# Performance work log

Hardware: AMD Instinct MI355X
Metric: run time of the kernel (lower is better)

The kernel has to match this reference:

```python
import jax, jax.numpy as jnp
import numpy as np
from math import factorial

LMAX = 4
L2 = (LMAX + 1) ** 2                      # 25 spherical components
RES_B = 2 * (2 * LMAX + 1)                # 18 Gauss-Legendre beta nodes (exact for band 2*lmax products)
RES_A = 2 * (2 * LMAX + 1) + 1            # 19 uniform alpha nodes
EPS = 1e-5
# degree index of each (l,m) slot: [0,1,1,1,2,...]
L_IDX = np.repeat(np.arange(LMAX + 1), 2 * np.arange(LMAX + 1) + 1)


def _assoc_legendre(lmax, x):
    # Associated Legendre P_l^m(x) with Condon-Shortley phase; returns [l, m, B]
    B = x.shape[0]
    P = np.zeros((lmax + 1, lmax + 1, B))
    P[0, 0] = 1.0
    sx = np.sqrt(np.maximum(0.0, 1.0 - x * x))
    for m in range(1, lmax + 1):
        P[m, m] = -(2 * m - 1) * sx * P[m - 1, m - 1]
    for m in range(lmax):
        P[m + 1, m] = (2 * m + 1) * x * P[m, m]
    for m in range(lmax + 1):
        for l in range(m + 2, lmax + 1):
            P[l, m] = ((2 * l - 1) * x * P[l - 1, m] - (l + m - 1) * P[l - 2, m]) / (l - m)
    return P


def _build_sh(lmax, res_b, res_a):
    # Real orthonormal spherical harmonics sampled on a Gauss-Legendre x uniform-phi grid.
    ct, wb = np.polynomial.legendre.leggauss(res_b)       # cos(theta) nodes / weights
    phi = np.arange(res_a) * (2.0 * np.pi / res_a)
    P = _assoc_legendre(lmax, ct)
    l2 = (lmax + 1) ** 2
    Y = np.zeros((res_b, res_a, l2))
    for l in range(lmax + 1):
        for m in range(l + 1):
            Nlm = np.sqrt((2 * l + 1) / (4.0 * np.pi) * factorial(l - m) / factorial(l + m))
            if m == 0:
                Y[:, :, l * l + l] = (Nlm * P[l, 0])[:, None]
            else:
                base = np.sqrt(2.0) * Nlm * P[l, m]
                Y[:, :, l * l + l + m] = base[:, None] * np.cos(m * phi)[None, :]
                Y[:, :, l * l + l - m] = base[:, None] * np.sin(m * phi)[None, :]
    w = (wb[:, None] * np.full((1, res_a), 2.0 * np.pi / res_a)).reshape(-1)
    Yf = Y.reshape(-1, l2)
    return Yf, w

_Y_np, _w_np = _build_sh(LMAX, RES_B, RES_A)
TO_GRID = jnp.asarray(_Y_np, dtype=jnp.float32)                     # [G, L2]
FROM_GRID = jnp.asarray((_w_np[:, None] * _Y_np).T, dtype=jnp.float32)  # [L2, G], exact SH projection


def setup_inputs() -> dict:
    key = jax.random.key(0)
    ks = jax.random.split(key, 8)
    N, C = 6000, 128
    x = jax.random.normal(ks[0], (N, L2, C), dtype=jnp.float32)
    batch = jax.random.randint(ks[1], (N,), 0, 77)
    s = 1.0 / np.sqrt(C)
    return {
        "x": x,
        "batch": batch,
        "norm_w": jnp.ones((LMAX + 1, C), dtype=jnp.float32),
        "norm_b": jnp.zeros((C,), dtype=jnp.float32),
        "w1": jax.random.normal(ks[2], (LMAX + 1, C, C), dtype=jnp.float32) * s,
        "b1": jax.random.normal(ks[3], (C,), dtype=jnp.float32) * 0.02,
        "w_tp": jax.random.normal(ks[4], (LMAX + 1, C), dtype=jnp.float32),
        "w2": jax.random.normal(ks[5], (LMAX + 1, C, C), dtype=jnp.float32) * s,
        "b2": jax.random.normal(ks[6], (C,), dtype=jnp.float32) * 0.02,
    }


def _merge_layer_norm(x, w, b):
    # x: [N, L2, C]; center l=0 over channels, RMS over all components+channels, per-(l,C) affine.
    mean0 = jnp.mean(x[:, 0:1, :], axis=-1, keepdims=True)
    xc = jnp.concatenate([x[:, 0:1, :] - mean0, x[:, 1:, :]], axis=1)
    var = jnp.mean(xc * xc, axis=(1, 2), keepdims=True)
    xn = xc * jax.lax.rsqrt(var + EPS)
    out = xn * w[L_IDX][None]                      # [N, L2, C]
    return jnp.concatenate([out[:, 0:1, :] + b, out[:, 1:, :]], axis=1)


def _so3_linear(x, w, b):
    # per-degree linear: w [lmax+1, out, in]; bias on l=0 only
    W = w[L_IDX]                                    # [L2, out, in]
    y = jnp.einsum('nlc,lkc->nlk', x, W)
    return jnp.concatenate([y[:, 0:1, :] + b, y[:, 1:, :]], axis=1)


def _gaunt_self_tp(x, w_tp):
    # Gaunt self tensor-product (depthwise): pointwise square on the sphere,
    # exact projection back to SH (Gaunt-coefficient contraction), per-(l,C) weight.
    g = jnp.einsum('nlc,gl->ngc', x, TO_GRID)       # [N, G, C] to-grid
    y = jnp.einsum('ngc,lg->nlc', g * g, FROM_GRID)  # [N, L2, C] from-grid
    return y * w_tp[L_IDX][None]


def reference(x, batch, norm_w, norm_b, w1, b1, w_tp, w2, b2):
    x_res = x
    h = _merge_layer_norm(x, norm_w, norm_b)
    h = _so3_linear(h, w1, b1)
    h = _gaunt_self_tp(h, w_tp)
    h = _so3_linear(h, w2, b2)
    return h + x_res  # ffn_shortcut is Identity (num_in == num_out)
```

## Files before the change

### kernel.cpp

```cpp
#include <hip/hip_runtime.h>
#include <math.h>

#define L2C 25
#define CH  128
#define NB  16
#define GLB 7
#define GLA 13
#define NG  91
#define GPAD 96
#define KPAD 32
#define HROWS 401

typedef short bf16x8 __attribute__((ext_vector_type(8)));
typedef int   i32x4  __attribute__((ext_vector_type(4)));
typedef float f32x4  __attribute__((ext_vector_type(4)));
typedef unsigned uint2v __attribute__((ext_vector_type(2)));

union frag_u { i32x4 i; bf16x8 h; };

__device__ inline short f2bf(float f) {
  union { float f; unsigned u; } v; v.f = f;
  unsigned r = (v.u + 0x7FFFu + ((v.u >> 16) & 1u)) >> 16;
  return (short)r;
}
__device__ inline unsigned cvt_pk_bf16(float lo, float hi) {
  unsigned r; asm("v_cvt_pk_bf16_f32 %0, %1, %2" : "=v"(r) : "v"(lo), "v"(hi)); return r;
}

__global__ void build_tables_kernel(short* __restrict__ toT, short* __restrict__ frT) {
  const int g = threadIdx.x;
  if (g >= GPAD) return;
  const double PI = 3.14159265358979323846;
  double Y[L2C];
  double wg = 0.0;
  if (g < NG) {
    const int b = g / GLA;
    const int a = g % GLA;
    double xx = cos(PI * (b + 0.75) / (GLB + 0.5));
    double pp = 1.0;
    for (int it = 0; it < 64; ++it) {
      double p0 = 1.0, p1 = xx;
      for (int j = 2; j <= GLB; ++j) { double p2 = ((2.0*j-1.0)*xx*p1 - (j-1.0)*p0)/j; p0 = p1; p1 = p2; }
      pp = GLB * (xx*p1 - p0) / (xx*xx - 1.0);
      xx -= p1 / pp;
    }
    { double p0 = 1.0, p1 = xx;
      for (int j = 2; j <= GLB; ++j) { double p2 = ((2.0*j-1.0)*xx*p1 - (j-1.0)*p0)/j; p0 = p1; p1 = p2; }
      pp = GLB * (xx*p1 - p0) / (xx*xx - 1.0); }
    const double wb = 2.0 / ((1.0 - xx*xx) * pp * pp);
    const double ct = xx;
    const double sx = sqrt(fmax(0.0, 1.0 - ct*ct));
    double P[5][5];
    P[0][0] = 1.0;
    for (int m = 1; m <= 4; ++m) P[m][m] = -(2.0*m - 1.0) * sx * P[m-1][m-1];
    for (int m = 0; m <= 3; ++m) P[m+1][m] = (2.0*m + 1.0) * ct * P[m][m];
    for (int m = 0; m <= 4; ++m)
      for (int l = m + 2; l <= 4; ++l)
        P[l][m] = ((2.0*l-1.0)*ct*P[l-1][m] - (l+m-1.0)*P[l-2][m]) / (l - m);
    const double fact[9] = {1,1,2,6,24,120,720,5040,40320};
    const double phi = (2.0*PI/GLA) * a;
    for (int l = 0; l <= 4; ++l)
      for (int m = 0; m <= l; ++m) {
        double Nlm = sqrt((2.0*l+1.0)/(4.0*PI) * fact[l-m]/fact[l+m]);
        if (m == 0) Y[l*l + l] = Nlm * P[l][0];
        else {
          double base = sqrt(2.0) * Nlm * P[l][m];
          Y[l*l + l + m] = base * cos((double)m * phi);
          Y[l*l + l - m] = base * sin((double)m * phi);
        }
      }
    wg = wb * (2.0*PI/GLA);
  }
  for (int l = 0; l < KPAD; ++l) {
    float tv = (g < NG && l < L2C) ? (float)Y[l] : 0.f;
    toT[g*KPAD + l] = f2bf(tv);
  }
  {
    const int hi = g >> 4, r = g & 15;
    const int ksv = hi >> 1, pa = hi & 1;
    const int lqv = r >> 2,  pb = r & 3;
    const int kg = ksv*32 + lqv*8 + pa*4 + pb;
    for (int l = 0; l < KPAD; ++l)
      frT[l*GPAD + kg] = (g < NG && l < L2C) ? f2bf((float)(wg * Y[l])) : (short)0;
  }
}

__global__ void convert_w_kernel(const float* __restrict__ w1, const float* __restrict__ w2,
                                 short* __restrict__ wb1, short* __restrict__ wb2) {
  const int i = blockIdx.x * 256 + threadIdx.x;
  if (i < 5*CH*CH) { wb1[i] = f2bf(w1[i]); wb2[i] = f2bf(w2[i]); }
}

__global__ __launch_bounds__(512, 2) void eqv3_fused16(
    const float* __restrict__ x,
    const float* __restrict__ norm_w, const float* __restrict__ norm_b,
    const short* __restrict__ wb1, const float* __restrict__ b1,
    const float* __restrict__ w_tp,
    const short* __restrict__ wb2, const float* __restrict__ b2,
    const short* __restrict__ toT, const short* __restrict__ frT,
    float* __restrict__ out)
{
  __shared__ __align__(16) short u[65536];
  short (*hsh)[HROWS][8] = (short (*)[HROWS][8])u;
  short (*hg)[4][CH][8]  = (short (*)[4][CH][8])u;

  const int tid  = threadIdx.x;
  const int w    = tid >> 6;
  const int lane = tid & 63;
  const int l16  = lane & 15;
  const int lq   = lane >> 4;
  const long n0  = (long)blockIdx.x * NB;
  const int k    = w*16 + l16;

  constexpr int LDEG[L2C] = {0,1,1,1,2,2,2,2,2,3,3,3,3,3,3,3,4,4,4,4,4,4,4,4,4};
  constexpr int NT[5]     = {1,3,5,7,9};

  #pragma unroll
  for (int rep = 0; rep < 2; ++rep) {
    const int node = w + rep*8;
    const float4* x4 = (const float4*)(x + (n0 + node)*(long)(L2C*CH));
    float4 xv[13];
    float s0 = 0.f, s0q = 0.f, sq = 0.f;
    #pragma unroll
    for (int it = 0; it < 13; ++it) {
      const int j = it*64 + lane;
      if (j < 800) {
        xv[it] = x4[j];
        const float t = xv[it].x*xv[it].x + xv[it].y*xv[it].y + xv[it].z*xv[it].z + xv[it].w*xv[it].w;
        if (j < 32) { s0 += xv[it].x + xv[it].y + xv[it].z + xv[it].w; s0q += t; }
        else        sq += t;
      }
    }
    #pragma unroll
    for (int o = 1; o < 64; o <<= 1) {
      s0  += __shfl_xor(s0,  o, 64);
      s0q += __shfl_xor(s0q, o, 64);
      sq  += __shfl_xor(sq,  o, 64);
    }
    const float mean0 = s0 * (1.f/CH);
    const float var   = (sq + s0q - CH*mean0*mean0) * (1.f/(L2C*CH));
    const float rstd  = rsqrtf(var + 1e-5f);
    #pragma unroll
    for (int it = 0; it < 13; ++it) {
      const int j = it*64 + lane;
      if (j < 800) {
        const int s = j >> 5;
        const int d = (int)sqrtf((float)s + 0.5f);
        const int row = 16*s + node;
        const int c32 = j & 31;
        const int c0  = c32 * 4;
        const float4 nw4 = ((const float4*)norm_w)[d*32 + c32];
        float a0 = xv[it].x, a1 = xv[it].y, a2 = xv[it].z, a3 = xv[it].w;
        if (s == 0) {
          const float4 nb4 = ((const float4*)norm_b)[c32];
          a0 = (a0 - mean0)*rstd*nw4.x + nb4.x;
          a1 = (a1 - mean0)*rstd*nw4.y + nb4.y;
          a2 = (a2 - mean0)*rstd*nw4.z + nb4.z;
          a3 = (a3 - mean0)*rstd*nw4.w + nb4.w;
        } else {
          a0 *= rstd*nw4.x; a1 *= rstd*nw4.y; a2 *= rstd*nw4.z; a3 *= rstd*nw4.w;
        }
        uint2v pk; pk[0] = cvt_pk_bf16(a0, a1); pk[1] = cvt_pk_bf16(a2, a3);
        *(uint2v*)&hsh[c0 >> 3][row][c0 & 7] = pk;
      }
    }
  }
  __syncthreads();

  unsigned pk1[L2C][2];
  {
    const float b1k = b1[k];
    int s = 0;
    #pragma unroll
    for (int d = 0; d < 5; ++d) {
      frag_u B[4];
      #pragma unroll
      for (int ks = 0; ks < 4; ++ks)
        B[ks].i = *(const i32x4*)(wb1 + ((d*CH + k)*CH + ks*32 + lq*8));
      #pragma unroll
      for (int mt = 0; mt < NT[d]; ++mt, ++s) {
        f32x4 acc = {0.f, 0.f, 0.f, 0.f};
        #pragma unroll
        for (int ks = 0; ks < 4; ++ks) {
          const bf16x8 a = *(const bf16x8*)&hsh[ks*4 + lq][16*s + l16][0];
          acc = __builtin_amdgcn_mfma_f32_16x16x32_bf16(a, B[ks].h, acc, 0, 0, 0);
        }
        const float bb = (s == 0) ? b1k : 0.f;
        pk1[s][0] = cvt_pk_bf16(acc[0] + bb, acc[1] + bb);
        pk1[s][1] = cvt_pk_bf16(acc[2] + bb, acc[3] + bb);
      }
    }
  }
  __syncthreads();

  {
    const i32x4 z = {0,0,0,0};
    #pragma unroll
    for (int j = 0; j < 4; ++j)
      *(i32x4*)&hg[lq*4 + j][3][k][0] = z;
    #pragma unroll
    for (int s = 0; s < L2C; ++s) {
      const int nb = lq*4;
      hg[nb+0][s >> 3][k][s & 7] = (short)(pk1[s][0] & 0xFFFFu);
      hg[nb+1][s >> 3][k][s & 7] = (short)(pk1[s][0] >> 16);
      hg[nb+2][s >> 3][k][s & 7] = (short)(pk1[s][1] & 0xFFFFu);
      hg[nb+3][s >> 3][k][s & 7] = (short)(pk1[s][1] >> 16);
    }
  }

  frag_u Bh[NB];
  #pragma unroll
  for (int n = 0; n < NB; ++n)
    Bh[n].i = *(const i32x4*)&hg[n][lq][k][0];
  __syncthreads();

  {
    frag_u Ato[6];
    #pragma unroll
    for (int gt = 0; gt < 6; ++gt)
      Ato[gt].i = *(const i32x4*)(toT + (gt*16 + l16)*KPAD + lq*8);
    frag_u Afr[2][3];
    #pragma unroll
    for (int mt = 0; mt < 2; ++mt)
      #pragma unroll
      for (int ks = 0; ks < 3; ++ks)
        Afr[mt][ks].i = *(const i32x4*)(frT + (mt*16 + l16)*GPAD + ks*32 + lq*8);

    float wtp[2][4]; int hrowb[2][4];
    #pragma unroll
    for (int mt = 0; mt < 2; ++mt)
      #pragma unroll
      for (int i = 0; i < 4; ++i) {
        const int l = mt*16 + lq*4 + i;
        if (l < L2C) {
          wtp[mt][i]   = w_tp[LDEG[l]*CH + k];
          hrowb[mt][i] = 16*l;
        } else { wtp[mt][i] = 0.f; hrowb[mt][i] = -1; }
      }

    #pragma unroll
    for (int np = 0; np < 8; ++np) {
      const int nA = np, nB2 = np + 8;
      unsigned pA[6][2], pB[6][2];
      #pragma unroll
      for (int gt = 0; gt < 6; ++gt) {
        f32x4 aA = {0.f,0.f,0.f,0.f}, aB = {0.f,0.f,0.f,0.f};
        aA = __builtin_amdgcn_mfma_f32_16x16x32_bf16(Ato[gt].h, Bh[nA].h,  aA, 0, 0, 0);
        aB = __builtin_amdgcn_mfma_f32_16x16x32_bf16(Ato[gt].h, Bh[nB2].h, aB, 0, 0, 0);
        pA[gt][0] = cvt_pk_bf16(aA[0]*aA[0], aA[1]*aA[1]);
        pA[gt][1] = cvt_pk_bf16(aA[2]*aA[2], aA[3]*aA[3]);
        pB[gt][0] = cvt_pk_bf16(aB[0]*aB[0], aB[1]*aB[1]);
        pB[gt][1] = cvt_pk_bf16(aB[2]*aB[2], aB[3]*aB[3]);
      }
      f32x4 acc2A[2] = {{0.f,0.f,0.f,0.f},{0.f,0.f,0.f,0.f}};
      f32x4 acc2B[2] = {{0.f,0.f,0.f,0.f},{0.f,0.f,0.f,0.f}};
      #pragma unroll
      for (int ks = 0; ks < 3; ++ks) {
        frag_u BgA, BgB;
        BgA.i[0] = (int)pA[2*ks][0];   BgA.i[1] = (int)pA[2*ks][1];
        BgA.i[2] = (int)pA[2*ks+1][0]; BgA.i[3] = (int)pA[2*ks+1][1];
        BgB.i[0] = (int)pB[2*ks][0];   BgB.i[1] = (int)pB[2*ks][1];
        BgB.i[2] = (int)pB[2*ks+1][0]; BgB.i[3] = (int)pB[2*ks+1][1];
        acc2A[0] = __builtin_amdgcn_mfma_f32_16x16x32_bf16(Afr[0][ks].h, BgA.h, acc2A[0], 0, 0, 0);
        acc2A[1] = __builtin_amdgcn_mfma_f32_16x16x32_bf16(Afr[1][ks].h, BgA.h, acc2A[1], 0, 0, 0);
        acc2B[0] = __builtin_amdgcn_mfma_f32_16x16x32_bf16(Afr[0][ks].h, BgB.h, acc2B[0], 0, 0, 0);
        acc2B[1] = __builtin_amdgcn_mfma_f32_16x16x32_bf16(Afr[1][ks].h, BgB.h, acc2B[1], 0, 0, 0);
      }
      #pragma unroll
      for (int mt = 0; mt < 2; ++mt)
        #pragma unroll
        for (int i = 0; i < 4; ++i)
          if (hrowb[mt][i] >= 0) {
            hsh[k >> 3][hrowb[mt][i] + nA][k & 7]  = f2bf(acc2A[mt][i] * wtp[mt][i]);
            hsh[k >> 3][hrowb[mt][i] + nB2][k & 7] = f2bf(acc2B[mt][i] * wtp[mt][i]);
          }
    }
  }
  __syncthreads();

  {
    const float b2k = b2[k];
    int s = 0;
    #pragma unroll
    for (int d = 0; d < 5; ++d) {
      frag_u B[4];
      #pragma unroll
      for (int ks = 0; ks < 4; ++ks)
        B[ks].i = *(const i32x4*)(wb2 + ((d*CH + k)*CH + ks*32 + lq*8));
      #pragma unroll
      for (int mt = 0; mt < NT[d]; ++mt, ++s) {
        f32x4 acc = {0.f, 0.f, 0.f, 0.f};
        #pragma unroll
        for (int ks = 0; ks < 4; ++ks) {
          const bf16x8 a = *(const bf16x8*)&hsh[ks*4 + lq][16*s + l16][0];
          acc = __builtin_amdgcn_mfma_f32_16x16x32_bf16(a, B[ks].h, acc, 0, 0, 0);
        }
        const float bb = (s == 0) ? b2k : 0.f;
        #pragma unroll
        for (int i = 0; i < 4; ++i) {
          const int node = lq*4 + i;
          const long base = (n0 + node)*(long)(L2C*CH) + s*CH + k;
          out[base] = acc[i] + bb + x[base];
        }
      }
    }
  }
}

extern "C" void kernel_launch(void* const* d_in, const int* in_sizes, int n_in,
                              void* d_out, int out_size, void* d_ws, size_t ws_size,
                              hipStream_t stream) {
  const float* x      = (const float*)d_in[0];
  const float* norm_w = (const float*)d_in[2];
  const float* norm_b = (const float*)d_in[3];
  const float* w1     = (const float*)d_in[4];
  const float* b1     = (const float*)d_in[5];
  const float* w_tp   = (const float*)d_in[6];
  const float* w2     = (const float*)d_in[7];
  const float* b2     = (const float*)d_in[8];
  float* out = (float*)d_out;

  const int N = in_sizes[0] / (L2C*CH);

  short* wsS = (short*)d_ws;
  short* toT = wsS;
  short* frT = toT + GPAD*KPAD;
  short* wb1 = frT + KPAD*GPAD;
  short* wb2 = wb1 + 5*CH*CH;

  build_tables_kernel<<<1, 128, 0, stream>>>(toT, frT);
  convert_w_kernel<<<(5*CH*CH + 255)/256, 256, 0, stream>>>(w1, w2, wb1, wb2);
  eqv3_fused16<<<N/NB, 512, 0, stream>>>(x, norm_w, norm_b, wb1, b1, w_tp, wb2, b2, toT, frT, out);
}
```

Baseline: 107.3 us.

## Double workgroup to 1024 threads, splitting node and SH-row work across wave halves

The fused kernel now runs 16 waves instead of 8. Each wave normalizes one node, and the two wave halves split the SH rows (0-12 and 13-24) in both per-degree linear layers and split the 16 nodes in the Gaunt grid stage. This halves per-thread register state (pk1, Bh, accumulators) and aims to raise latency hiding and occupancy, though the 128KB LDS per block may still cap residency. The Gauss-Legendre Newton iteration count in the table builder also drops from 64 to 5, trimming setup-kernel time.

```diff
diff --git a/kernel.cpp b/kernel.cpp
--- a/kernel.cpp
+++ b/kernel.cpp
@@ -38,7 +38,7 @@
     const int a = g % GLA;
     double xx = cos(PI * (b + 0.75) / (GLB + 0.5));
     double pp = 1.0;
-    for (int it = 0; it < 64; ++it) {
+    for (int it = 0; it < 5; ++it) {
       double p0 = 1.0, p1 = xx;
       for (int j = 2; j <= GLB; ++j) { double p2 = ((2.0*j-1.0)*xx*p1 - (j-1.0)*p0)/j; p0 = p1; p1 = p2; }
       pp = GLB * (xx*p1 - p0) / (xx*xx - 1.0);
@@ -91,7 +91,7 @@
   if (i < 5*CH*CH) { wb1[i] = f2bf(w1[i]); wb2[i] = f2bf(w2[i]); }
 }
 
-__global__ __launch_bounds__(512, 2) void eqv3_fused16(
+__global__ __launch_bounds__(1024, 4) void eqv3_fused16w(
     const float* __restrict__ x,
     const float* __restrict__ norm_w, const float* __restrict__ norm_b,
     const short* __restrict__ wb1, const float* __restrict__ b1,
@@ -106,18 +106,18 @@
 
   const int tid  = threadIdx.x;
   const int w    = tid >> 6;
+  const int kw   = w & 7;
+  const int hw   = w >> 3;
   const int lane = tid & 63;
   const int l16  = lane & 15;
   const int lq   = lane >> 4;
   const long n0  = (long)blockIdx.x * NB;
-  const int k    = w*16 + l16;
+  const int k    = kw*16 + l16;
 
   constexpr int LDEG[L2C] = {0,1,1,1,2,2,2,2,2,3,3,3,3,3,3,3,4,4,4,4,4,4,4,4,4};
-  constexpr int NT[5]     = {1,3,5,7,9};
-
-  #pragma unroll
-  for (int rep = 0; rep < 2; ++rep) {
-    const int node = w + rep*8;
+
+  {
+    const int node = w;
     const float4* x4 = (const float4*)(x + (n0 + node)*(long)(L2C*CH));
     float4 xv[13];
     float s0 = 0.f, s0q = 0.f, sq = 0.f;
@@ -167,143 +167,139 @@
   }
   __syncthreads();
 
-  unsigned pk1[L2C][2];
-  {
-    const float b1k = b1[k];
-    int s = 0;
-    #pragma unroll
-    for (int d = 0; d < 5; ++d) {
-      frag_u B[4];
-      #pragma unroll
-      for (int ks = 0; ks < 4; ++ks)
-        B[ks].i = *(const i32x4*)(wb1 + ((d*CH + k)*CH + ks*32 + lq*8));
-      #pragma unroll
-      for (int mt = 0; mt < NT[d]; ++mt, ++s) {
-        f32x4 acc = {0.f, 0.f, 0.f, 0.f};
-        #pragma unroll
-        for (int ks = 0; ks < 4; ++ks) {
-          const bf16x8 a = *(const bf16x8*)&hsh[ks*4 + lq][16*s + l16][0];
-          acc = __builtin_amdgcn_mfma_f32_16x16x32_bf16(a, B[ks].h, acc, 0, 0, 0);
-        }
-        const float bb = (s == 0) ? b1k : 0.f;
-        pk1[s][0] = cvt_pk_bf16(acc[0] + bb, acc[1] + bb);
-        pk1[s][1] = cvt_pk_bf16(acc[2] + bb, acc[3] + bb);
-      }
-    }
-  }
-  __syncthreads();
-
-  {
-    const i32x4 z = {0,0,0,0};
-    #pragma unroll
-    for (int j = 0; j < 4; ++j)
-      *(i32x4*)&hg[lq*4 + j][3][k][0] = z;
-    #pragma unroll
-    for (int s = 0; s < L2C; ++s) {
-      const int nb = lq*4;
-      hg[nb+0][s >> 3][k][s & 7] = (short)(pk1[s][0] & 0xFFFFu);
-      hg[nb+1][s >> 3][k][s & 7] = (short)(pk1[s][0] >> 16);
-      hg[nb+2][s >> 3][k][s & 7] = (short)(pk1[s][1] & 0xFFFFu);
-      hg[nb+3][s >> 3][k][s & 7] = (short)(pk1[s][1] >> 16);
-    }
-  }
-
-  frag_u Bh[NB];
+  unsigned pk1[13][2];
+  const float b1k = b1[k];
+#define L1SEG(D, S0, S1, SB) { \
+    frag_u Bf[4]; \
+    _Pragma("unroll") for (int ks = 0; ks < 4; ++ks) \
+      Bf[ks].i = *(const i32x4*)(wb1 + (((D)*CH + k)*CH + ks*32 + lq*8)); \
+    _Pragma("unroll") for (int s = (S0); s < (S1); ++s) { \
+      f32x4 acc = {0.f,0.f,0.f,0.f}; \
+      _Pragma("unroll") for (int ks = 0; ks < 4; ++ks) { \
+        const bf16x8 a = *(const bf16x8*)&hsh[ks*4 + lq][16*s + l16][0]; \
+        acc = __builtin_amdgcn_mfma_f32_16x16x32_bf16(a, Bf[ks].h, acc, 0, 0, 0); } \
+      const float bb = (s == 0) ? b1k : 0.f; \
+      pk1[s - (SB)][0] = cvt_pk_bf16(acc[0] + bb, acc[1] + bb); \
+      pk1[s - (SB)][1] = cvt_pk_bf16(acc[2] + bb, acc[3] + bb); } }
+  if (hw == 0) {
+    L1SEG(0, 0, 1, 0); L1SEG(1, 1, 4, 0); L1SEG(2, 4, 9, 0); L1SEG(3, 9, 13, 0);
+  } else {
+    L1SEG(3, 13, 16, 13); L1SEG(4, 16, 25, 13);
+  }
+#undef L1SEG
+  __syncthreads();
+
+  frag_u Ato[6];
   #pragma unroll
-  for (int n = 0; n < NB; ++n)
-    Bh[n].i = *(const i32x4*)&hg[n][lq][k][0];
-  __syncthreads();
-
-  {
-    frag_u Ato[6];
-    #pragma unroll
-    for (int gt = 0; gt < 6; ++gt)
-      Ato[gt].i = *(const i32x4*)(toT + (gt*16 + l16)*KPAD + lq*8);
-    frag_u Afr[2][3];
-    #pragma unroll
-    for (int mt = 0; mt < 2; ++mt)
-      #pragma unroll
-      for (int ks = 0; ks < 3; ++ks)
-        Afr[mt][ks].i = *(const i32x4*)(frT + (mt*16 + l16)*GPAD + ks*32 + lq*8);
-
-    float wtp[2][4]; int hrowb[2][4];
-    #pragma unroll
-    for (int mt = 0; mt < 2; ++mt)
-      #pragma unroll
-      for (int i = 0; i < 4; ++i) {
-        const int l = mt*16 + lq*4 + i;
-        if (l < L2C) {
-          wtp[mt][i]   = w_tp[LDEG[l]*CH + k];
-          hrowb[mt][i] = 16*l;
-        } else { wtp[mt][i] = 0.f; hrowb[mt][i] = -1; }
-      }
-
-    #pragma unroll
-    for (int np = 0; np < 8; ++np) {
-      const int nA = np, nB2 = np + 8;
-      unsigned pA[6][2], pB[6][2];
+  for (int gt = 0; gt < 6; ++gt)
+    Ato[gt].i = *(const i32x4*)(toT + (gt*16 + l16)*KPAD + lq*8);
+  frag_u Afr[2][3];
+  #pragma unroll
+  for (int mt = 0; mt < 2; ++mt)
+    #pragma unroll
+    for (int ks = 0; ks < 3; ++ks)
+      Afr[mt][ks].i = *(const i32x4*)(frT + (mt*16 + l16)*GPAD + ks*32 + lq*8);
+  float wtp[2][4]; int hrowb[2][4];
+  #pragma unroll
+  for (int mt = 0; mt < 2; ++mt)
+    #pragma unroll
+    for (int i = 0; i < 4; ++i) {
+      const int l = mt*16 + lq*4 + i;
+      if (l < L2C) {
+        wtp[mt][i]   = w_tp[LDEG[l]*CH + k];
+        hrowb[mt][i] = 16*l;
+      } else { wtp[mt][i] = 0.f; hrowb[mt][i] = -1; }
+    }
+
+  {
+    if (hw == 1) {
+      const i32x4 z = {0,0,0,0};
+      #pragma unroll
+      for (int j = 0; j < 4; ++j)
+        *(i32x4*)&hg[lq*4 + j][3][k][0] = z;
+    }
+    const int nb = lq*4;
+    if (hw == 0) {
+      #pragma unroll
+      for (int s = 0; s < 13; ++s) {
+        hg[nb+0][s >> 3][k][s & 7] = (short)(pk1[s][0] & 0xFFFFu);
+        hg[nb+1][s >> 3][k][s & 7] = (short)(pk1[s][0] >> 16);
+        hg[nb+2][s >> 3][k][s & 7] = (short)(pk1[s][1] & 0xFFFFu);
+        hg[nb+3][s >> 3][k][s & 7] = (short)(pk1[s][1] >> 16);
+      }
+    } else {
+      #pragma unroll
+      for (int s = 13; s < 25; ++s) {
+        hg[nb+0][s >> 3][k][s & 7] = (short)(pk1[s-13][0] & 0xFFFFu);
+        hg[nb+1][s >> 3][k][s & 7] = (short)(pk1[s-13][0] >> 16);
+        hg[nb+2][s >> 3][k][s & 7] = (short)(pk1[s-13][1] & 0xFFFFu);
+        hg[nb+3][s >> 3][k][s & 7] = (short)(pk1[s-13][1] >> 16);
+      }
+    }
+  }
+  __syncthreads();
+
+  frag_u Bh[8];
+  #pragma unroll
+  for (int j = 0; j < 8; ++j)
+    Bh[j].i = *(const i32x4*)&hg[hw*8 + j][lq][k][0];
+  __syncthreads();
+
+  {
+    #pragma unroll
+    for (int j = 0; j < 8; ++j) {
+      const int n = hw*8 + j;
+      unsigned p[6][2];
       #pragma unroll
       for (int gt = 0; gt < 6; ++gt) {
-        f32x4 aA = {0.f,0.f,0.f,0.f}, aB = {0.f,0.f,0.f,0.f};
-        aA = __builtin_amdgcn_mfma_f32_16x16x32_bf16(Ato[gt].h, Bh[nA].h,  aA, 0, 0, 0);
-        aB = __builtin_amdgcn_mfma_f32_16x16x32_bf16(Ato[gt].h, Bh[nB2].h, aB, 0, 0, 0);
-        pA[gt][0] = cvt_pk_bf16(aA[0]*aA[0], aA[1]*aA[1]);
-        pA[gt][1] = cvt_pk_bf16(aA[2]*aA[2], aA[3]*aA[3]);
-        pB[gt][0] = cvt_pk_bf16(aB[0]*aB[0], aB[1]*aB[1]);
-        pB[gt][1] = cvt_pk_bf16(aB[2]*aB[2], aB[3]*aB[3]);
-      }
-      f32x4 acc2A[2] = {{0.f,0.f,0.f,0.f},{0.f,0.f,0.f,0.f}};
-      f32x4 acc2B[2] = {{0.f,0.f,0.f,0.f},{0.f,0.f,0.f,0.f}};
+        f32x4 acc = {0.f,0.f,0.f,0.f};
+        acc = __builtin_amdgcn_mfma_f32_16x16x32_bf16(Ato[gt].h, Bh[j].h, acc, 0, 0, 0);
+        p[gt][0] = cvt_pk_bf16(acc[0]*acc[0], acc[1]*acc[1]);
+        p[gt][1] = cvt_pk_bf16(acc[2]*acc[2], acc[3]*acc[3]);
+      }
+      f32x4 acc2[2] = {{0.f,0.f,0.f,0.f},{0.f,0.f,0.f,0.f}};
       #pragma unroll
       for (int ks = 0; ks < 3; ++ks) {
-        frag_u BgA, BgB;
-        BgA.i[0] = (int)pA[2*ks][0];   BgA.i[1] = (int)pA[2*ks][1];
-        BgA.i[2] = (int)pA[2*ks+1][0]; BgA.i[3] = (int)pA[2*ks+1][1];
-        BgB.i[0] = (int)pB[2*ks][0];   BgB.i[1] = (int)pB[2*ks][1];
-        BgB.i[2] = (int)pB[2*ks+1][0]; BgB.i[3] = (int)pB[2*ks+1][1];
-        acc2A[0] = __builtin_amdgcn_mfma_f32_16x16x32_bf16(Afr[0][ks].h, BgA.h, acc2A[0], 0, 0, 0);
-        acc2A[1] = __builtin_amdgcn_mfma_f32_16x16x32_bf16(Afr[1][ks].h, BgA.h, acc2A[1], 0, 0, 0);
-        acc2B[0] = __builtin_amdgcn_mfma_f32_16x16x32_bf16(Afr[0][ks].h, BgB.h, acc2B[0], 0, 0, 0);
-        acc2B[1] = __builtin_amdgcn_mfma_f32_16x16x32_bf16(Afr[1][ks].h, BgB.h, acc2B[1], 0, 0, 0);
+        frag_u Bg;
+        Bg.i[0] = (int)p[2*ks][0];
+        Bg.i[1] = (int)p[2*ks][1];
+        Bg.i[2] = (int)p[2*ks+1][0];
+        Bg.i[3] = (int)p[2*ks+1][1];
+        acc2[0] = __builtin_amdgcn_mfma_f32_16x16x32_bf16(Afr[0][ks].h, Bg.h, acc2[0], 0, 0, 0);
+        acc2[1] = __builtin_amdgcn_mfma_f32_16x16x32_bf16(Afr[1][ks].h, Bg.h, acc2[1], 0, 0, 0);
       }
       #pragma unroll
       for (int mt = 0; mt < 2; ++mt)
         #pragma unroll
         for (int i = 0; i < 4; ++i)
-          if (hrowb[mt][i] >= 0) {
-            hsh[k >> 3][hrowb[mt][i] + nA][k & 7]  = f2bf(acc2A[mt][i] * wtp[mt][i]);
-            hsh[k >> 3][hrowb[mt][i] + nB2][k & 7] = f2bf(acc2B[mt][i] * wtp[mt][i]);
-          }
+          if (hrowb[mt][i] >= 0)
+            hsh[k >> 3][hrowb[mt][i] + n][k & 7] = f2bf(acc2[mt][i] * wtp[mt][i]);
     }
   }
   __syncthreads();
 
   {
     const float b2k = b2[k];
-    int s = 0;
-    #pragma unroll
-    for (int d = 0; d < 5; ++d) {
-      frag_u B[4];
-      #pragma unroll
-      for (int ks = 0; ks < 4; ++ks)
-        B[ks].i = *(const i32x4*)(wb2 + ((d*CH + k)*CH + ks*32 + lq*8));
-      #pragma unroll
-      for (int mt = 0; mt < NT[d]; ++mt, ++s) {
-        f32x4 acc = {0.f, 0.f, 0.f, 0.f};
-        #pragma unroll
-        for (int ks = 0; ks < 4; ++ks) {
-          const bf16x8 a = *(const bf16x8*)&hsh[ks*4 + lq][16*s + l16][0];
-          acc = __builtin_amdgcn_mfma_f32_16x16x32_bf16(a, B[ks].h, acc, 0, 0, 0);
-        }
-        const float bb = (s == 0) ? b2k : 0.f;
-        #pragma unroll
-        for (int i = 0; i < 4; ++i) {
-          const int node = lq*4 + i;
-          const long base = (n0 + node)*(long)(L2C*CH) + s*CH + k;
-          out[base] = acc[i] + bb + x[base];
-        }
-      }
-    }
+#define L2SEG(D, S0, S1) { \
+    frag_u Bf[4]; \
+    _Pragma("unroll") for (int ks = 0; ks < 4; ++ks) \
+      Bf[ks].i = *(const i32x4*)(wb2 + (((D)*CH + k)*CH + ks*32 + lq*8)); \
+    _Pragma("unroll") for (int s = (S0); s < (S1); ++s) { \
+      f32x4 acc = {0.f,0.f,0.f,0.f}; \
+      _Pragma("unroll") for (int ks = 0; ks < 4; ++ks) { \
+        const bf16x8 a = *(const bf16x8*)&hsh[ks*4 + lq][16*s + l16][0]; \
+        acc = __builtin_amdgcn_mfma_f32_16x16x32_bf16(a, Bf[ks].h, acc, 0, 0, 0); } \
+      const float bb = (s == 0) ? b2k : 0.f; \
+      _Pragma("unroll") for (int i = 0; i < 4; ++i) { \
+        const int node = lq*4 + i; \
+        const long base = (n0 + node)*(long)(L2C*CH) + s*CH + k; \
+        out[base] = acc[i] + bb + x[base]; } } }
+    if (hw == 0) {
+      L2SEG(0, 0, 1); L2SEG(1, 1, 4); L2SEG(2, 4, 9); L2SEG(3, 9, 13);
+    } else {
+      L2SEG(3, 13, 16); L2SEG(4, 16, 25);
+    }
+#undef L2SEG
   }
 }
 
@@ -330,5 +326,5 @@
 
   build_tables_kernel<<<1, 128, 0, stream>>>(toT, frT);
   convert_w_kernel<<<(5*CH*CH + 255)/256, 256, 0, stream>>>(w1, w2, wb1, wb2);
-  eqv3_fused16<<<N/NB, 512, 0, stream>>>(x, norm_w, norm_b, wb1, b1, w_tp, wb2, b2, toT, frT, out);
-}
+  eqv3_fused16w<<<N/NB, 1024, 0, stream>>>(x, norm_w, norm_b, wb1, b1, w_tp, wb2, b2, toT, frT, out);
+}
```

After: 221.6 us. 2.07x slower.
